# Performance work log

Hardware: AMD Instinct MI355X
Metric: run time of the kernel (lower is better)

The kernel has to match this reference:

```python
import jax, jax.numpy as jnp
import numpy as np

D_MODEL = 512
KEY_DIM = 512
VALUE_DIM = 512
N_HEADS = 8


def setup_inputs() -> dict:
    key = jax.random.key(0)
    ks = jax.random.split(key, 12)
    B, S = 8, 1024
    s = 0.02
    return {
        "input1": jax.random.normal(ks[0], (B, S, D_MODEL), jnp.float32),
        "input2": jax.random.normal(ks[1], (B, S, D_MODEL), jnp.float32),
        "input3": jax.random.normal(ks[2], (B, S, D_MODEL), jnp.float32),
        # per-head projection weights stacked over heads: [H, D, d]
        "Wq": jax.random.normal(ks[3], (N_HEADS, D_MODEL, KEY_DIM), jnp.float32) * s,
        "bq": jnp.zeros((N_HEADS, KEY_DIM), jnp.float32),
        "Wk": jax.random.normal(ks[4], (N_HEADS, D_MODEL, KEY_DIM), jnp.float32) * s,
        "bk": jnp.zeros((N_HEADS, KEY_DIM), jnp.float32),
        "Wv": jax.random.normal(ks[5], (N_HEADS, D_MODEL, VALUE_DIM), jnp.float32) * s,
        "bv": jnp.zeros((N_HEADS, VALUE_DIM), jnp.float32),
        # output projection: concat of heads (H*VALUE_DIM) -> KEY_DIM
        "Wo": jax.random.normal(ks[6], (N_HEADS * VALUE_DIM, KEY_DIM), jnp.float32) * s,
        "bo": jnp.zeros((KEY_DIM,), jnp.float32),
    }


def reference(input1, input2, input3, Wq, bq, Wk, bk, Wv, bv, Wo, bo):
    # Batched equivalent of the per-head Python loop:
    # each head: q=Dense_q(input1), k=Dense_k(input2), v=Dense_v(input3);
    # softmax(q k^T / sqrt(key_dim)) v; concat over heads; Dense w_o.
    q = jnp.einsum("bsd,hde->bhse", input1, Wq) + bq[None, :, None, :]
    k = jnp.einsum("bsd,hde->bhse", input2, Wk) + bk[None, :, None, :]
    v = jnp.einsum("bsd,hde->bhse", input3, Wv) + bv[None, :, None, :]
    scale = 1.0 / jnp.sqrt(jnp.asarray(KEY_DIM, q.dtype))
    scores = jnp.einsum("bhqe,bhke->bhqk", q, k) * scale  # [B,H,S,S]
    attn = jax.nn.softmax(scores, axis=-1)
    heads = jnp.einsum("bhqk,bhke->bhqe", attn, v)  # [B,H,S,VALUE_DIM]
    B, H, S, E = heads.shape
    concat = jnp.transpose(heads, (0, 2, 1, 3)).reshape(B, S, H * E)
    return concat @ Wo + bo
```

## Files before the change

### kernel.cpp

```cpp
#include <hip/hip_runtime.h>
#include <hip/hip_bf16.h>

#define DEV static __device__ __forceinline__

typedef float f32x4 __attribute__((ext_vector_type(4)));
typedef __bf16 b16x8 __attribute__((ext_vector_type(8)));

DEV unsigned short f2bf(float f) {
  union { __hip_bfloat16 h; unsigned short u; } cv;
  cv.h = __float2bfloat16(f);
  return cv.u;
}

DEV void gload_lds16(const unsigned short* g, unsigned short* l) {
  __builtin_amdgcn_global_load_lds(
      (__attribute__((address_space(1))) void*)g,
      (__attribute__((address_space(3))) void*)l, 16, 0, 0);
}

__global__ __launch_bounds__(256) void k_convall(
    const float* __restrict__ in1, const float* __restrict__ in2,
    const float* __restrict__ in3, const float* __restrict__ Wq,
    const float* __restrict__ Wk,
    unsigned short* __restrict__ in1b, unsigned short* __restrict__ in2b,
    unsigned short* __restrict__ in3b, unsigned short* __restrict__ wqb,
    unsigned short* __restrict__ wkb) {
  const int b = blockIdx.x;
  const float* src;
  unsigned short* dst;
  long long off;
  if (b < 4096) { src = in1; dst = in1b; off = b; }
  else if (b < 8192) { src = in2; dst = in2b; off = b - 4096; }
  else if (b < 12288) { src = in3; dst = in3b; off = b - 8192; }
  else if (b < 14336) { src = Wq; dst = wqb; off = b - 12288; }
  else { src = Wk; dst = wkb; off = b - 14336; }
  const long long i = off * 256 + threadIdx.x;
  const float4 v = ((const float4*)src)[i];
  ushort4 o;
  o.x = f2bf(v.x); o.y = f2bf(v.y); o.z = f2bf(v.z); o.w = f2bf(v.w);
  ((ushort4*)dst)[i] = o;
}

__global__ __launch_bounds__(256) void k_transall(const float* __restrict__ Wv,
                                                  const float* __restrict__ Wo,
                                                  unsigned short* __restrict__ wvt,
                                                  unsigned short* __restrict__ wot) {
  __shared__ float t[32][33];
  const int yy = blockIdx.y;
  const float* src;
  unsigned short* dst;
  long long zo;
  int R, C, r0;
  const int c0 = blockIdx.x * 32;
  if (yy < 128) {
    src = Wv; dst = wvt; R = 512; C = 512;
    zo = (long long)(yy >> 4) * 512 * 512;
    r0 = (yy & 15) * 32;
  } else {
    src = Wo; dst = wot; R = 4096; C = 512;
    zo = 0;
    r0 = (yy - 128) * 32;
  }
  const int tx = threadIdx.x & 31, ty = threadIdx.x >> 5;
#pragma unroll
  for (int i = 0; i < 4; ++i)
    t[ty + i * 8][tx] = src[zo + (long long)(r0 + ty + i * 8) * C + c0 + tx];
  __syncthreads();
#pragma unroll
  for (int i = 0; i < 4; ++i)
    dst[zo + (long long)(c0 + ty + i * 8) * R + r0 + tx] = f2bf(t[tx][ty + i * 8]);
}

__global__ __launch_bounds__(256) void k_uv(const float* __restrict__ Wq, const float* __restrict__ bk,
                                            const float* __restrict__ Wk, const float* __restrict__ bq,
                                            float* __restrict__ u, float* __restrict__ v) {
  const int sel = blockIdx.y;
  const float* W = sel ? Wk : Wq;
  const float* bb = sel ? bq : bk;
  float* dst = sel ? v : u;
  const int wave = threadIdx.x >> 6, lane = threadIdx.x & 63;
  const int idx = blockIdx.x * 4 + wave;
  const int h = idx >> 9, d = idx & 511;
  const float* wr = W + ((long long)h * 512 + d) * 512 + lane * 8;
  const float* br = bb + h * 512 + lane * 8;
  float s = 0.f;
#pragma unroll
  for (int k = 0; k < 8; ++k) s += wr[k] * br[k];
#pragma unroll
  for (int off = 32; off; off >>= 1) s += __shfl_xor(s, off);
  if (lane == 0) dst[h * 512 + d] = s;
}

__global__ __launch_bounds__(512) void k_bdot(const float* __restrict__ bq,
                                              const float* __restrict__ bk,
                                              float* __restrict__ c) {
  const int wave = threadIdx.x >> 6, lane = threadIdx.x & 63;
  const float* a = bq + wave * 512 + lane * 8;
  const float* b = bk + wave * 512 + lane * 8;
  float s = 0.f;
#pragma unroll
  for (int k = 0; k < 8; ++k) s += a[k] * b[k];
#pragma unroll
  for (int off = 32; off; off >>= 1) s += __shfl_xor(s, off);
  if (lane == 0) c[wave] = s;
}

__global__ __launch_bounds__(256) void k_rtct(const float* __restrict__ in1, const float* __restrict__ in2,
                                              const float* __restrict__ u, const float* __restrict__ v,
                                              const float* __restrict__ cbuf,
                                              float* __restrict__ rt, float* __restrict__ ct) {
  const int sel = blockIdx.y;
  const float* src = sel ? in2 : in1;
  const float* vec = sel ? v : u;
  float* dst = sel ? ct : rt;
  const int row = blockIdx.x;
  __shared__ float x[512];
  const float* p = src + (long long)row * 512;
  x[threadIdx.x] = p[threadIdx.x];
  x[threadIdx.x + 256] = p[threadIdx.x + 256];
  __syncthreads();
  const int wave = threadIdx.x >> 6, lane = threadIdx.x & 63;
  const int b = row >> 10, i = row & 1023;
#pragma unroll
  for (int t = 0; t < 2; ++t) {
    const int h = wave * 2 + t;
    const float* wv = vec + h * 512;
    float s = 0.f;
#pragma unroll
    for (int k = 0; k < 8; ++k) s += x[lane + k * 64] * wv[lane + k * 64];
#pragma unroll
    for (int off = 32; off; off >>= 1) s += __shfl_xor(s, off);
    if (lane == 0)
      dst[((long long)(b * 8 + h)) * 1024 + i] = s + (sel ? 0.f : cbuf[h]);
  }
}

__global__ __launch_bounds__(256) void k_softmax_bf16(unsigned short* __restrict__ P) {
  const int wave = threadIdx.x >> 6, lane = threadIdx.x & 63;
  unsigned short* p = P + ((long long)blockIdx.x * 4 + wave) * 1024 + lane * 16;
  const b16x8 v0 = *(const b16x8*)p;
  const b16x8 v1 = *(const b16x8*)(p + 8);
  float f[16];
#pragma unroll
  for (int j = 0; j < 8; ++j) { f[j] = (float)v0[j]; f[8 + j] = (float)v1[j]; }
  float mx = f[0];
#pragma unroll
  for (int j = 1; j < 16; ++j) mx = fmaxf(mx, f[j]);
#pragma unroll
  for (int off = 32; off; off >>= 1) mx = fmaxf(mx, __shfl_xor(mx, off));
  float sum = 0.f;
#pragma unroll
  for (int j = 0; j < 16; ++j) { f[j] = __expf(f[j] - mx); sum += f[j]; }
#pragma unroll
  for (int off = 32; off; off >>= 1) sum += __shfl_xor(sum, off);
  const float inv = 1.f / sum;
  b16x8 o0, o1;
#pragma unroll
  for (int j = 0; j < 8; ++j) { o0[j] = (__bf16)(f[j] * inv); o1[j] = (__bf16)(f[8 + j] * inv); }
  *(b16x8*)p = o0;
  *(b16x8*)(p + 8) = o1;
}

template <int OM>
__global__ __launch_bounds__(256) void k_gemm_bt(
    const unsigned short* __restrict__ A, const unsigned short* __restrict__ Bt,
    void* __restrict__ Cv, const float* __restrict__ bias,
    const float* __restrict__ rAdd, const float* __restrict__ cAdd,
    int K, int lda, int ldb, int ldc,
    int azs, int azm, long long azr,
    int bzs, int bzm, long long bzr,
    int czs, long long czr, int czm, int czc,
    int biasm, int bstr, int rstr, float scale) {
  __shared__ unsigned short lA[128 * 64];
  __shared__ unsigned short lB[128 * 64];
  const int tid = threadIdx.x, wave = tid >> 6, lane = tid & 63;
  const int z = blockIdx.z;
  const int m0 = blockIdx.y * 128, n0 = blockIdx.x * 128;
  const unsigned short* Az = A + (long long)((z >> azs) & azm) * azr + (long long)m0 * lda;
  const unsigned short* Bz = Bt + (long long)((z >> bzs) & bzm) * bzr + (long long)n0 * ldb;

  const int srow = wave * 32 + (lane >> 3);
  const int scol = (lane & 7) * 8;
  const unsigned short* ga = Az + (long long)srow * lda + scol;
  const unsigned short* gb = Bz + (long long)srow * ldb + scol;
  unsigned short* laBase = &lA[(wave * 32) * 64];
  unsigned short* lbBase = &lB[(wave * 32) * 64];

  f32x4 acc[4][4] = {};
  const int wr = (wave >> 1) * 64, wc = (wave & 1) * 64;
  const int fr = lane & 15, kq = (lane >> 4) * 8;

  for (int k0 = 0; k0 < K; k0 += 64) {
#pragma unroll
    for (int i = 0; i < 4; ++i) {
      gload_lds16(ga + (long long)(i * 8) * lda + k0, laBase + (i * 8) * 64);
      gload_lds16(gb + (long long)(i * 8) * ldb + k0, lbBase + (i * 8) * 64);
    }
    __syncthreads();
#pragma unroll
    for (int kk = 0; kk < 64; kk += 32) {
      b16x8 af[4], bf[4];
#pragma unroll
      for (int i = 0; i < 4; ++i)
        af[i] = *(const b16x8*)&lA[(wr + i * 16 + fr) * 64 + kk + kq];
#pragma unroll
      for (int j = 0; j < 4; ++j)
        bf[j] = *(const b16x8*)&lB[(wc + j * 16 + fr) * 64 + kk + kq];
#pragma unroll
      for (int i = 0; i < 4; ++i)
#pragma unroll
        for (int j = 0; j < 4; ++j)
          acc[i][j] = __builtin_amdgcn_mfma_f32_16x16x32_bf16(af[i], bf[j], acc[i][j], 0, 0, 0);
    }
    __syncthreads();
  }

  const long long coff = (long long)(z >> czs) * czr + (long long)(z & czm) * czc;
  const long long zr = (long long)z * rstr;
  const int rr = (lane >> 4) * 4;
#pragma unroll
  for (int j = 0; j < 4; ++j) {
    const int col = n0 + wc + j * 16 + fr;
    const float bval = bias ? bias[(long long)(z & biasm) * bstr + col] : 0.f;
    const float ca = cAdd ? cAdd[zr + col] : 0.f;
#pragma unroll
    for (int i = 0; i < 4; ++i) {
#pragma unroll
      for (int r = 0; r < 4; ++r) {
        const int row = m0 + wr + i * 16 + rr + r;
        const float ra = rAdd ? rAdd[zr + row] : 0.f;
        const float val = (acc[i][j][r] + ra + ca) * scale + bval;
        if constexpr (OM == 1) {
          ((unsigned short*)Cv)[coff + (long long)row * ldc + col] = f2bf(val);
        } else if constexpr (OM == 2) {
          ((unsigned short*)Cv)[coff + (long long)col * ldc + row] = f2bf(val);
        } else {
          ((float*)Cv)[coff + (long long)row * ldc + col] = val;
        }
      }
    }
  }
}

#define STAGE_A8(nb, koff, i)                                  \
  gload_lds16(gaL + (long long)((i) * 8) * lda + (koff) + scol, \
              &sh[nb][(wid * 32 + (i) * 8) * 64])
#define STAGE_B8(nb, koff, i)                                  \
  gload_lds16(gbL + (long long)((i) * 8) * ldb + (koff) + scol, \
              &sh[2 + (nb)][(wid * 32 + (i) * 8) * 64])

template <int OM>
__global__ __launch_bounds__(512, 2) void k_gemm8p(
    const unsigned short* __restrict__ A, const unsigned short* __restrict__ Bt,
    void* __restrict__ Cv, const float* __restrict__ bias,
    const float* __restrict__ rAdd, const float* __restrict__ cAdd,
    int K, int lda, int ldb, int ldc,
    int azs, int azm, long long azr,
    int bzs, int bzm, long long bzr,
    int czs, long long czr, int czm, int czc,
    int biasm, int bstr, int rstr, float scale, int kzm, int kzr) {
  __shared__ unsigned short sh[4][256 * 64];
  const int tid = threadIdx.x, wid = tid >> 6, lane = tid & 63;
  const int wm = wid >> 2, wn = wid & 3;

  const int gx = gridDim.x, gy = gridDim.y;
  const int nwg = gx * gy * gridDim.z;
  const int bidL = blockIdx.x + gx * (blockIdx.y + gy * blockIdx.z);
  const int q8 = nwg >> 3;
  const int idx = (bidL & 7) * q8 + (bidL >> 3);
  const int bx = idx % gx;
  const int rem = idx / gx;
  const int by = rem % gy;
  const int z = rem / gy;

  const int m0 = by * 256, n0 = bx * 256;
  const int kstart = (z & kzm) * kzr;
  const unsigned short* Az = A + (long long)((z >> azs) & azm) * azr + (long long)m0 * lda + kstart;
  const unsigned short* Bz = Bt + (long long)((z >> bzs) & bzm) * bzr + (long long)n0 * ldb + kstart;

  const int scol = (((lane & 7) ^ ((lane >> 3) & 7)) << 3);
  const unsigned short* gaL = Az + (long long)(wid * 32 + (lane >> 3)) * lda;
  const unsigned short* gbL = Bz + (long long)(wid * 32 + (lane >> 3)) * ldb;

  const int fr = lane & 15, kq = (lane >> 4) * 8;
  const int fsw = (fr & 7) << 3;
  const int rc0 = kq ^ fsw;
  const int rc1 = (32 + kq) ^ fsw;
  const int aBase = (wm * 128 + fr) * 64;
  const int bBase = (wn * 64 + fr) * 64;

  f32x4 acc[8][4] = {};
  b16x8 afr[4][2], bfr[4][2];
  const int NT = K >> 6;

#pragma unroll
  for (int i = 0; i < 4; ++i) { STAGE_A8(0, 0, i); STAGE_B8(0, 0, i); }

  for (int kt = 0; kt < NT; ++kt) {
    const int cur = kt & 1, nb = cur ^ 1;
    if (kt + 1 < NT) {
      const int ko = (kt + 1) << 6;
#pragma unroll
      for (int i = 0; i < 4; ++i) { STAGE_A8(nb, ko, i); STAGE_B8(nb, ko, i); }
      asm volatile("s_waitcnt vmcnt(8)" ::: "memory");
    } else {
      asm volatile("s_waitcnt vmcnt(0)" ::: "memory");
    }
    __builtin_amdgcn_s_barrier();
    __builtin_amdgcn_sched_barrier(0);

#pragma unroll
    for (int i = 0; i < 4; ++i) {
      afr[i][0] = *(const b16x8*)&sh[cur][aBase + i * 1024 + rc0];
      afr[i][1] = *(const b16x8*)&sh[cur][aBase + i * 1024 + rc1];
    }
#pragma unroll
    for (int j = 0; j < 2; ++j) {
      bfr[j][0] = *(const b16x8*)&sh[2 + cur][bBase + j * 1024 + rc0];
      bfr[j][1] = *(const b16x8*)&sh[2 + cur][bBase + j * 1024 + rc1];
    }
    __builtin_amdgcn_s_setprio(1);
#pragma unroll
    for (int t = 0; t < 2; ++t)
#pragma unroll
      for (int i = 0; i < 4; ++i)
#pragma unroll
        for (int j = 0; j < 2; ++j)
          acc[i][j] = __builtin_amdgcn_mfma_f32_16x16x32_bf16(afr[i][t], bfr[j][t], acc[i][j], 0, 0, 0);
    __builtin_amdgcn_s_setprio(0);
#pragma unroll
    for (int j = 2; j < 4; ++j) {
      bfr[j][0] = *(const b16x8*)&sh[2 + cur][bBase + j * 1024 + rc0];
      bfr[j][1] = *(const b16x8*)&sh[2 + cur][bBase + j * 1024 + rc1];
    }
    __builtin_amdgcn_s_setprio(1);
#pragma unroll
    for (int t = 0; t < 2; ++t)
#pragma unroll
      for (int i = 0; i < 4; ++i)
#pragma unroll
        for (int j = 2; j < 4; ++j)
          acc[i][j] = __builtin_amdgcn_mfma_f32_16x16x32_bf16(afr[i][t], bfr[j][t], acc[i][j], 0, 0, 0);
    __builtin_amdgcn_s_setprio(0);
#pragma unroll
    for (int i = 0; i < 4; ++i) {
      afr[i][0] = *(const b16x8*)&sh[cur][aBase + (i + 4) * 1024 + rc0];
      afr[i][1] = *(const b16x8*)&sh[cur][aBase + (i + 4) * 1024 + rc1];
    }
    __builtin_amdgcn_s_setprio(1);
#pragma unroll
    for (int t = 0; t < 2; ++t)
#pragma unroll
      for (int i = 0; i < 4; ++i)
#pragma unroll
        for (int j = 0; j < 2; ++j)
          acc[i + 4][j] = __builtin_amdgcn_mfma_f32_16x16x32_bf16(afr[i][t], bfr[j][t], acc[i + 4][j], 0, 0, 0);
    __builtin_amdgcn_s_setprio(0);
    __builtin_amdgcn_s_setprio(1);
#pragma unroll
    for (int t = 0; t < 2; ++t)
#pragma unroll
      for (int i = 0; i < 4; ++i)
#pragma unroll
        for (int j = 2; j < 4; ++j)
          acc[i + 4][j] = __builtin_amdgcn_mfma_f32_16x16x32_bf16(afr[i][t], bfr[j][t], acc[i + 4][j], 0, 0, 0);
    __builtin_amdgcn_s_setprio(0);

    __builtin_amdgcn_s_barrier();
  }

  const long long coff = (long long)(z >> czs) * czr + (long long)(z & czm) * czc;
  const long long zr = (long long)z * rstr;
  const int rr = (lane >> 4) * 4;
  unsigned short* flat = &sh[0][0];

#pragma unroll
  for (int j = 0; j < 4; ++j) {
    const int col = n0 + wn * 64 + j * 16 + fr;
    const float bval = bias ? bias[(long long)(z & biasm) * bstr + col] : 0.f;
    const float ca = cAdd ? cAdd[zr + col] : 0.f;
#pragma unroll
    for (int i = 0; i < 8; ++i) {
#pragma unroll
      for (int r = 0; r < 4; ++r) {
        const int row = m0 + wm * 128 + i * 16 + rr + r;
        const float ra = rAdd ? rAdd[zr + row] : 0.f;
        const float val = (acc[i][j][r] + ra + ca) * scale + bval;
        const int rowL = wm * 128 + i * 16 + rr + r;
        const int colL = wn * 64 + j * 16 + fr;
        const int sR = (OM == 2) ? colL : rowL;
        const int sC = (OM == 2) ? rowL : colL;
        flat[sR * 256 + (sC ^ ((sR & 7) << 3))] = f2bf(val);
      }
    }
  }
  __builtin_amdgcn_s_barrier();
  const long long rbase = (OM == 2) ? (long long)n0 : (long long)m0;
  const long long cbase = (OM == 2) ? (long long)m0 : (long long)n0;
  unsigned short* Cb = (unsigned short*)Cv;
#pragma unroll
  for (int it = 0; it < 16; ++it) {
    const int t = it * 512 + tid;
    const int R = t >> 5;
    const int Cq = t & 31;
    const int q = Cq ^ (R & 7);
    const b16x8 v = *(const b16x8*)&flat[R * 256 + q * 8];
    *(b16x8*)(Cb + coff + (rbase + R) * ldc + cbase + Cq * 8) = v;
  }
}

#define STAGE_GA(nb, koff, i)                                  \
  gload_lds16(gaL + (long long)((i) * 8) * lda + (koff) + scol, \
              &sh[nb][(wid * 32 + (i) * 8) * 64])
#define STAGE_GB(nb, koff, i)                                  \
  gload_lds16(gbL + (long long)((i) * 8) * ldb + (koff) + scol, \
              &sh[2 + (nb)][(wid * 32 + (i) * 8) * 64])

template <int OM>
__global__ __launch_bounds__(256, 2) void k_g128(
    const unsigned short* __restrict__ A, const unsigned short* __restrict__ Bt,
    void* __restrict__ Cv, const float* __restrict__ bias,
    const float* __restrict__ rAdd, const float* __restrict__ cAdd,
    int K, int lda, int ldb, int ldc,
    int azs, int azm, long long azr,
    int bzs, int bzm, long long bzr,
    int czs, long long czr, int czm, int czc,
    int biasm, int bstr, int rstr, float scale, int kzm, int kzr) {
  __shared__ unsigned short sh[4][128 * 64];
  const int tid = threadIdx.x, wid = tid >> 6, lane = tid & 63;
  const int wm = wid >> 1, wn = wid & 1;

  const int gx = gridDim.x, gy = gridDim.y;
  const int nwg = gx * gy * gridDim.z;
  const int bidL = blockIdx.x + gx * (blockIdx.y + gy * blockIdx.z);
  const int q8 = nwg >> 3;
  const int idx = (bidL & 7) * q8 + (bidL >> 3);
  const int bx = idx % gx;
  const int rem = idx / gx;
  const int by = rem % gy;
  const int z = rem / gy;

  const int m0 = by * 128, n0 = bx * 128;
  const int kstart = (z & kzm) * kzr;
  const unsigned short* Az = A + (long long)((z >> azs) & azm) * azr + (long long)m0 * lda + kstart;
  const unsigned short* Bz = Bt + (long long)((z >> bzs) & bzm) * bzr + (long long)n0 * ldb + kstart;

  const int scol = (((lane & 7) ^ ((lane >> 3) & 7)) << 3);
  const unsigned short* gaL = Az + (long long)(wid * 32 + (lane >> 3)) * lda;
  const unsigned short* gbL = Bz + (long long)(wid * 32 + (lane >> 3)) * ldb;

  const int fr = lane & 15, kq = (lane >> 4) * 8;
  const int fsw = (fr & 7) << 3;
  const int rc0 = kq ^ fsw;
  const int rc1 = (32 + kq) ^ fsw;
  const int aBase = (wm * 64 + fr) * 64;
  const int bBase = (wn * 64 + fr) * 64;

  f32x4 acc[4][4] = {};
  b16x8 afr[4][2], bfr[4][2];
  const int NT = K >> 6;

#pragma unroll
  for (int i = 0; i < 4; ++i) { STAGE_GA(0, 0, i); STAGE_GB(0, 0, i); }

  for (int kt = 0; kt < NT; ++kt) {
    const int cur = kt & 1, nb = cur ^ 1;
    if (kt + 1 < NT) {
      const int ko = (kt + 1) << 6;
#pragma unroll
      for (int i = 0; i < 4; ++i) { STAGE_GA(nb, ko, i); STAGE_GB(nb, ko, i); }
      asm volatile("s_waitcnt vmcnt(8)" ::: "memory");
    } else {
      asm volatile("s_waitcnt vmcnt(0)" ::: "memory");
    }
    __builtin_amdgcn_s_barrier();
    __builtin_amdgcn_sched_barrier(0);

#pragma unroll
    for (int i = 0; i < 4; ++i) {
      afr[i][0] = *(const b16x8*)&sh[cur][aBase + i * 1024 + rc0];
      afr[i][1] = *(const b16x8*)&sh[cur][aBase + i * 1024 + rc1];
    }
#pragma unroll
    for (int j = 0; j < 4; ++j) {
      bfr[j][0] = *(const b16x8*)&sh[2 + cur][bBase + j * 1024 + rc0];
      bfr[j][1] = *(const b16x8*)&sh[2 + cur][bBase + j * 1024 + rc1];
    }
#pragma unroll
    for (int t = 0; t < 2; ++t)
#pragma unroll
      for (int i = 0; i < 4; ++i)
#pragma unroll
        for (int j = 0; j < 4; ++j)
          acc[i][j] = __builtin_amdgcn_mfma_f32_16x16x32_bf16(afr[i][t], bfr[j][t], acc[i][j], 0, 0, 0);

    __builtin_amdgcn_s_barrier();
  }

  const long long coff = (long long)(z >> czs) * czr + (long long)(z & czm) * czc;
  const long long zr = (long long)z * rstr;
  const int rr = (lane >> 4) * 4;
  unsigned short* flat = &sh[0][0];

  if constexpr (OM == 1 || OM == 2) {
#pragma unroll
    for (int j = 0; j < 4; ++j) {
      const int col = n0 + wn * 64 + j * 16 + fr;
      const float bval = bias ? bias[(long long)(z & biasm) * bstr + col] : 0.f;
      const float ca = cAdd ? cAdd[zr + col] : 0.f;
#pragma unroll
      for (int i = 0; i < 4; ++i) {
#pragma unroll
        for (int r = 0; r < 4; ++r) {
          const int row = m0 + wm * 64 + i * 16 + rr + r;
          const float ra = rAdd ? rAdd[zr + row] : 0.f;
          const float val = (acc[i][j][r] + ra + ca) * scale + bval;
          const int rowL = wm * 64 + i * 16 + rr + r;
          const int colL = wn * 64 + j * 16 + fr;
          const int sR = (OM == 2) ? colL : rowL;
          const int sC = (OM == 2) ? rowL : colL;
          flat[sR * 128 + (sC ^ ((sR & 7) << 3))] = f2bf(val);
        }
      }
    }
    __builtin_amdgcn_s_barrier();
    const long long rbase = (OM == 2) ? (long long)n0 : (long long)m0;
    const long long cbase = (OM == 2) ? (long long)m0 : (long long)n0;
    unsigned short* Cb = (unsigned short*)Cv;
#pragma unroll
    for (int it = 0; it < 8; ++it) {
      const int t = it * 256 + tid;
      const int R = t >> 4;
      const int Cq = t & 15;
      const int q = Cq ^ (R & 7);
      const b16x8 v = *(const b16x8*)&flat[R * 128 + q * 8];
      *(b16x8*)(Cb + coff + (rbase + R) * ldc + cbase + Cq * 8) = v;
    }
  } else {
    float* fflat = (float*)flat;
    float* Cf = (float*)Cv;
#pragma unroll
    for (int j = 0; j < 4; ++j) {
      const int col = n0 + wn * 64 + j * 16 + fr;
      const float bval = bias ? bias[(long long)(z & biasm) * bstr + col] : 0.f;
      const float ca = cAdd ? cAdd[zr + col] : 0.f;
#pragma unroll
      for (int i = 0; i < 4; ++i) {
#pragma unroll
        for (int r = 0; r < 4; ++r) {
          const int row = m0 + wm * 64 + i * 16 + rr + r;
          const float ra = rAdd ? rAdd[zr + row] : 0.f;
          const float val = (acc[i][j][r] + ra + ca) * scale + bval;
          const int Rl = wm * 64 + i * 16 + rr + r;
          const int Cl = wn * 64 + j * 16 + fr;
          fflat[Rl * 128 + (Cl ^ ((Rl & 7) << 2))] = val;
        }
      }
    }
    __builtin_amdgcn_s_barrier();
#pragma unroll
    for (int it = 0; it < 16; ++it) {
      const int t = it * 256 + tid;
      const int R = t >> 5;
      const int Cq = t & 31;
      const int q = Cq ^ (R & 7);
      const float4 v = *(const float4*)&fflat[R * 128 + q * 4];
      *(float4*)(Cf + coff + (long long)(m0 + R) * ldc + n0 + Cq * 4) = v;
    }
  }
}

extern "C" void kernel_launch(void* const* d_in, const int* in_sizes, int n_in,
                              void* d_out, int out_size, void* d_ws, size_t ws_size,
                              hipStream_t stream) {
  const float* in1 = (const float*)d_in[0];
  const float* in2 = (const float*)d_in[1];
  const float* in3 = (const float*)d_in[2];
  const float* Wq = (const float*)d_in[3];
  const float* bq = (const float*)d_in[4];
  const float* Wk = (const float*)d_in[5];
  const float* bk = (const float*)d_in[6];
  const float* Wv = (const float*)d_in[7];
  const float* bv = (const float*)d_in[8];
  const float* Wo = (const float*)d_in[9];
  const float* bo = (const float*)d_in[10];

  const long long MB = 1024 * 1024;
  typedef unsigned short us;
  unsigned char* w = (unsigned char*)d_ws;
  us* in2b = (us*)(w);
  us* Tbuf = (us*)(w + 8 * MB);
  us* Vt = (us*)(w + 72 * MB);
  us* wvt = (us*)(w + 136 * MB);
  us* wot = (us*)(w + 140 * MB);
  us* scb = (us*)(w + 144 * MB);
  us* in1b = (us*)(w + 208 * MB);
  us* in3b = (us*)(w + 216 * MB);
  us* wqb = (us*)(w + 224 * MB);
  us* wkb = (us*)(w + 228 * MB);
  us* Gt = (us*)(w + 232 * MB);
  float* rt = (float*)(w + 236 * MB);
  float* ct = (float*)(w + 236 * MB + (256 << 10));
  float* ubuf = (float*)(w + 237 * MB);
  float* vbuf = (float*)(w + 237 * MB + (16 << 10));
  float* cbuf = (float*)(w + 237 * MB + (32 << 10));
  if ((long long)ws_size < 238 * MB) return;

  const float iscale = 0.04419417382415922f;
  const long long SD = 1024 * 512;

  k_convall<<<16384, 256, 0, stream>>>(in1, in2, in3, Wq, Wk,
                                       in1b, in2b, in3b, wqb, wkb);
  k_transall<<<dim3(16, 256), 256, 0, stream>>>(Wv, Wo, wvt, wot);

  k_uv<<<dim3(1024, 2), 256, 0, stream>>>(Wq, bk, Wk, bq, ubuf, vbuf);
  k_bdot<<<1, 512, 0, stream>>>(bq, bk, cbuf);
  k_rtct<<<dim3(8192, 2), 256, 0, stream>>>(in1, in2, ubuf, vbuf, cbuf, rt, ct);

  k_gemm_bt<1><<<dim3(4, 4, 8), 256, 0, stream>>>(
      wkb, wqb, Gt, nullptr, nullptr, nullptr, 512, 512, 512, 512,
      0, 7, 262144LL, 0, 7, 262144LL, 0, 262144LL, 0, 0, 0, 0, 0, 1.f);

  k_gemm8p<1><<<dim3(2, 4, 64), 512, 0, stream>>>(
      in1b, Gt, Tbuf, nullptr, nullptr, nullptr, 512, 512, 512, 512,
      3, 7, SD, 0, 7, 262144LL, 0, SD, 0, 0, 0, 0, 0, 1.f, 0, 0);

  k_gemm8p<2><<<dim3(2, 4, 64), 512, 0, stream>>>(
      in3b, wvt, Vt, bv, nullptr, nullptr, 512, 512, 512, 1024,
      3, 7, SD, 0, 7, 262144LL, 0, SD, 0, 0, 7, 512, 0, 1.f, 0, 0);

  for (int c = 0; c < 2; ++c) {
    k_gemm8p<1><<<dim3(4, 4, 32), 512, 0, stream>>>(
        Tbuf + (long long)c * 32 * SD, in2b + (long long)c * 4 * SD, scb, nullptr,
        rt + c * 32768, ct + c * 32768, 512, 512, 512, 1024,
        0, 31, SD, 3, 3, SD, 0, 1048576LL, 0, 0, 0, 0, 1024, iscale, 0, 0);
    k_softmax_bf16<<<8192, 256, 0, stream>>>(scb);
    k_gemm8p<1><<<dim3(2, 4, 32), 512, 0, stream>>>(
        scb, Vt + (long long)c * 32 * SD, Tbuf + (long long)c * 16777216LL, nullptr,
        nullptr, nullptr, 1024, 1024, 1024, 4096,
        0, 31, 1048576LL, 0, 31, SD, 3, 4194304LL, 7, 512, 0, 0, 0, 1.f, 0, 0);
  }

  k_g128<0><<<dim3(4, 64, 1), 256, 0, stream>>>(
      Tbuf, wot, d_out, bo, nullptr, nullptr, 4096, 4096, 4096, 512,
      0, 0, 0, 0, 0, 0, 0, 0, 0, 0, 0, 0, 0, 1.f, 0, 0);
}
```

Before: 465.0 us.

## Fuse QK^T, softmax and PV into a single attention kernel

Replaces the chunked sequence of score GEMM, separate bf16 softmax and PV GEMM with one k_attn kernel. Each block computes a 64-row query tile's full 1024-wide score row in registers, does a cross-wave softmax via LDS, stores the probabilities in LDS and multiplies by V, writing the concatenated head output directly. This removes the round trip of the B*H*S*S score matrix through global memory and several launches. In exchange it uses large LDS (160KB), limiting occupancy, and the PV loop loads V without double buffering.

```diff
diff --git a/kernel.cpp b/kernel.cpp
--- a/kernel.cpp
+++ b/kernel.cpp
@@ -135,32 +135,6 @@
   }
 }
 
-__global__ __launch_bounds__(256) void k_softmax_bf16(unsigned short* __restrict__ P) {
-  const int wave = threadIdx.x >> 6, lane = threadIdx.x & 63;
-  unsigned short* p = P + ((long long)blockIdx.x * 4 + wave) * 1024 + lane * 16;
-  const b16x8 v0 = *(const b16x8*)p;
-  const b16x8 v1 = *(const b16x8*)(p + 8);
-  float f[16];
-#pragma unroll
-  for (int j = 0; j < 8; ++j) { f[j] = (float)v0[j]; f[8 + j] = (float)v1[j]; }
-  float mx = f[0];
-#pragma unroll
-  for (int j = 1; j < 16; ++j) mx = fmaxf(mx, f[j]);
-#pragma unroll
-  for (int off = 32; off; off >>= 1) mx = fmaxf(mx, __shfl_xor(mx, off));
-  float sum = 0.f;
-#pragma unroll
-  for (int j = 0; j < 16; ++j) { f[j] = __expf(f[j] - mx); sum += f[j]; }
-#pragma unroll
-  for (int off = 32; off; off >>= 1) sum += __shfl_xor(sum, off);
-  const float inv = 1.f / sum;
-  b16x8 o0, o1;
-#pragma unroll
-  for (int j = 0; j < 8; ++j) { o0[j] = (__bf16)(f[j] * inv); o1[j] = (__bf16)(f[8 + j] * inv); }
-  *(b16x8*)p = o0;
-  *(b16x8*)(p + 8) = o1;
-}
-
 template <int OM>
 __global__ __launch_bounds__(256) void k_gemm_bt(
     const unsigned short* __restrict__ A, const unsigned short* __restrict__ Bt,
@@ -406,6 +380,228 @@
     const int q = Cq ^ (R & 7);
     const b16x8 v = *(const b16x8*)&flat[R * 256 + q * 8];
     *(b16x8*)(Cb + coff + (rbase + R) * ldc + cbase + Cq * 8) = v;
+  }
+}
+
+__global__ __launch_bounds__(512, 2) void k_attn(
+    const unsigned short* __restrict__ T, const unsigned short* __restrict__ X2,
+    const unsigned short* __restrict__ Vt,
+    const float* __restrict__ rt, const float* __restrict__ ct,
+    unsigned short* __restrict__ Cout, float iscale) {
+  __shared__ unsigned short sh[81920];
+  const int tid = threadIdx.x, wid = tid >> 6, lane = tid & 63;
+  const int bidL = blockIdx.x + 16 * blockIdx.y;
+  const int idx = (bidL & 7) * 128 + (bidL >> 3);
+  const int qt = idx & 15, z = idx >> 4;
+  const int b = z >> 3, h = z & 7;
+
+  const unsigned short* Tz = T + (long long)z * 524288 + (long long)qt * 64 * 512;
+  const unsigned short* Xb = X2 + (long long)b * 524288;
+  const unsigned short* Vz = Vt + (long long)z * 524288;
+
+  const int fr = lane & 15;
+  const int kq4 = lane >> 4;
+  const int rr = kq4 * 4;
+  const int srow4 = lane >> 2;
+  const int sq = (((lane & 3) ^ ((lane >> 2) & 3)) << 3);
+
+  f32x4 acc1[4][8] = {};
+  {
+#pragma unroll
+    for (int ii = 0; ii < 8; ++ii)
+      gload_lds16(Xb + (long long)(wid * 128 + ii * 16 + srow4) * 512 + sq,
+                  &sh[4096 + (wid * 128 + ii * 16) * 32 + lane * 8]);
+    if (wid < 4)
+      gload_lds16(Tz + (long long)(wid * 16 + srow4) * 512 + sq,
+                  &sh[(wid * 16) * 32 + lane * 8]);
+  }
+  for (int kt = 0; kt < 16; ++kt) {
+    const int cur = kt & 1, nb = cur ^ 1;
+    if (kt < 15) {
+      const int ko = (kt + 1) * 32;
+#pragma unroll
+      for (int ii = 0; ii < 8; ++ii)
+        gload_lds16(Xb + (long long)(wid * 128 + ii * 16 + srow4) * 512 + ko + sq,
+                    &sh[4096 + nb * 32768 + (wid * 128 + ii * 16) * 32 + lane * 8]);
+      if (wid < 4) {
+        gload_lds16(Tz + (long long)(wid * 16 + srow4) * 512 + ko + sq,
+                    &sh[nb * 2048 + (wid * 16) * 32 + lane * 8]);
+        asm volatile("s_waitcnt vmcnt(9)" ::: "memory");
+      } else {
+        asm volatile("s_waitcnt vmcnt(8)" ::: "memory");
+      }
+    } else {
+      asm volatile("s_waitcnt vmcnt(0)" ::: "memory");
+    }
+    __builtin_amdgcn_s_barrier();
+    __builtin_amdgcn_sched_barrier(0);
+    const int aB = cur * 2048, bB = 4096 + cur * 32768;
+    b16x8 af[4], bf[8];
+#pragma unroll
+    for (int i = 0; i < 4; ++i) {
+      const int row = i * 16 + fr;
+      af[i] = *(const b16x8*)&sh[aB + row * 32 + ((kq4 ^ (row & 3)) << 3)];
+    }
+#pragma unroll
+    for (int j = 0; j < 8; ++j) {
+      const int n = wid * 128 + j * 16 + fr;
+      bf[j] = *(const b16x8*)&sh[bB + n * 32 + ((kq4 ^ (n & 3)) << 3)];
+    }
+    __builtin_amdgcn_s_setprio(1);
+#pragma unroll
+    for (int i = 0; i < 4; ++i)
+#pragma unroll
+      for (int j = 0; j < 8; ++j)
+        acc1[i][j] = __builtin_amdgcn_mfma_f32_16x16x32_bf16(af[i], bf[j], acc1[i][j], 0, 0, 0);
+    __builtin_amdgcn_s_setprio(0);
+    __builtin_amdgcn_s_barrier();
+  }
+
+  float ca[8];
+#pragma unroll
+  for (int j = 0; j < 8; ++j) ca[j] = ct[(long long)z * 1024 + wid * 128 + j * 16 + fr];
+  float ra[4][4];
+#pragma unroll
+  for (int i = 0; i < 4; ++i)
+#pragma unroll
+    for (int r = 0; r < 4; ++r)
+      ra[i][r] = rt[(long long)z * 1024 + qt * 64 + i * 16 + rr + r];
+#pragma unroll
+  for (int i = 0; i < 4; ++i)
+#pragma unroll
+    for (int j = 0; j < 8; ++j)
+#pragma unroll
+      for (int r = 0; r < 4; ++r)
+        acc1[i][j][r] = (acc1[i][j][r] + ra[i][r] + ca[j]) * iscale;
+
+  float* sred = (float*)&sh[69632];
+  float* ssum = (float*)&sh[70656];
+  float rmax[4][4];
+#pragma unroll
+  for (int i = 0; i < 4; ++i)
+#pragma unroll
+    for (int r = 0; r < 4; ++r) {
+      float m = acc1[i][0][r];
+#pragma unroll
+      for (int j = 1; j < 8; ++j) m = fmaxf(m, acc1[i][j][r]);
+#pragma unroll
+      for (int off = 1; off < 16; off <<= 1) m = fmaxf(m, __shfl_xor(m, off));
+      rmax[i][r] = m;
+    }
+  if (fr == 0) {
+#pragma unroll
+    for (int i = 0; i < 4; ++i)
+#pragma unroll
+      for (int r = 0; r < 4; ++r) sred[wid * 64 + i * 16 + rr + r] = rmax[i][r];
+  }
+  __syncthreads();
+#pragma unroll
+  for (int i = 0; i < 4; ++i)
+#pragma unroll
+    for (int r = 0; r < 4; ++r) {
+      float m = sred[i * 16 + rr + r];
+#pragma unroll
+      for (int w = 1; w < 8; ++w) m = fmaxf(m, sred[w * 64 + i * 16 + rr + r]);
+      rmax[i][r] = m;
+    }
+  float rsum[4][4];
+#pragma unroll
+  for (int i = 0; i < 4; ++i)
+#pragma unroll
+    for (int r = 0; r < 4; ++r) {
+      float s = 0.f;
+#pragma unroll
+      for (int j = 0; j < 8; ++j) {
+        const float v = __expf(acc1[i][j][r] - rmax[i][r]);
+        acc1[i][j][r] = v;
+        s += v;
+      }
+#pragma unroll
+      for (int off = 1; off < 16; off <<= 1) s += __shfl_xor(s, off);
+      rsum[i][r] = s;
+    }
+  __syncthreads();
+  if (fr == 0) {
+#pragma unroll
+    for (int i = 0; i < 4; ++i)
+#pragma unroll
+      for (int r = 0; r < 4; ++r) ssum[wid * 64 + i * 16 + rr + r] = rsum[i][r];
+  }
+  __syncthreads();
+#pragma unroll
+  for (int i = 0; i < 4; ++i)
+#pragma unroll
+    for (int r = 0; r < 4; ++r) {
+      float s = ssum[i * 16 + rr + r];
+#pragma unroll
+      for (int w = 1; w < 8; ++w) s += ssum[w * 64 + i * 16 + rr + r];
+      rsum[i][r] = 1.f / s;
+    }
+#pragma unroll
+  for (int i = 0; i < 4; ++i)
+#pragma unroll
+    for (int j = 0; j < 8; ++j)
+#pragma unroll
+      for (int r = 0; r < 4; ++r) {
+        const int row = i * 16 + rr + r;
+        const int col = wid * 128 + j * 16 + fr;
+        sh[row * 1024 + ((((col >> 3) ^ (row & 7)) << 3) | (col & 7))] =
+            f2bf(acc1[i][j][r] * rsum[i][r]);
+      }
+  __syncthreads();
+
+  f32x4 acc2[4][4] = {};
+  for (int kt = 0; kt < 32; ++kt) {
+#pragma unroll
+    for (int ii = 0; ii < 4; ++ii)
+      gload_lds16(Vz + (long long)(wid * 64 + ii * 16 + srow4) * 1024 + kt * 32 + sq,
+                  &sh[65536 + (wid * 64 + ii * 16) * 32 + lane * 8]);
+    asm volatile("s_waitcnt vmcnt(0)" ::: "memory");
+    __builtin_amdgcn_s_barrier();
+    __builtin_amdgcn_sched_barrier(0);
+    b16x8 pa[4], vb[4];
+#pragma unroll
+    for (int i = 0; i < 4; ++i) {
+      const int row = i * 16 + fr;
+      const int q = kt * 4 + kq4;
+      pa[i] = *(const b16x8*)&sh[row * 1024 + ((q ^ (row & 7)) << 3)];
+    }
+#pragma unroll
+    for (int j = 0; j < 4; ++j) {
+      const int e = wid * 64 + j * 16 + fr;
+      vb[j] = *(const b16x8*)&sh[65536 + e * 32 + ((kq4 ^ (e & 3)) << 3)];
+    }
+    __builtin_amdgcn_s_setprio(1);
+#pragma unroll
+    for (int i = 0; i < 4; ++i)
+#pragma unroll
+      for (int j = 0; j < 4; ++j)
+        acc2[i][j] = __builtin_amdgcn_mfma_f32_16x16x32_bf16(pa[i], vb[j], acc2[i][j], 0, 0, 0);
+    __builtin_amdgcn_s_setprio(0);
+    __builtin_amdgcn_s_barrier();
+  }
+
+#pragma unroll
+  for (int i = 0; i < 4; ++i)
+#pragma unroll
+    for (int j = 0; j < 4; ++j)
+#pragma unroll
+      for (int r = 0; r < 4; ++r) {
+        const int row = i * 16 + rr + r;
+        const int col = wid * 64 + j * 16 + fr;
+        sh[row * 512 + ((((col >> 3) ^ (row & 7)) << 3) | (col & 7))] =
+            f2bf(acc2[i][j][r]);
+      }
+  __syncthreads();
+  unsigned short* Crow = Cout + (long long)(b * 1024 + qt * 64) * 4096 + h * 512;
+#pragma unroll
+  for (int it = 0; it < 8; ++it) {
+    const int t = it * 512 + tid;
+    const int R = t >> 6;
+    const int Cq = t & 63;
+    const int q = Cq ^ (R & 7);
+    const b16x8 v = *(const b16x8*)&sh[R * 512 + q * 8];
+    *(b16x8*)(Crow + (long long)R * 4096 + Cq * 8) = v;
   }
 }
 
@@ -629,19 +825,9 @@
       in3b, wvt, Vt, bv, nullptr, nullptr, 512, 512, 512, 1024,
       3, 7, SD, 0, 7, 262144LL, 0, SD, 0, 0, 7, 512, 0, 1.f, 0, 0);
 
-  for (int c = 0; c < 2; ++c) {
-    k_gemm8p<1><<<dim3(4, 4, 32), 512, 0, stream>>>(
-        Tbuf + (long long)c * 32 * SD, in2b + (long long)c * 4 * SD, scb, nullptr,
-        rt + c * 32768, ct + c * 32768, 512, 512, 512, 1024,
-        0, 31, SD, 3, 3, SD, 0, 1048576LL, 0, 0, 0, 0, 1024, iscale, 0, 0);
-    k_softmax_bf16<<<8192, 256, 0, stream>>>(scb);
-    k_gemm8p<1><<<dim3(2, 4, 32), 512, 0, stream>>>(
-        scb, Vt + (long long)c * 32 * SD, Tbuf + (long long)c * 16777216LL, nullptr,
-        nullptr, nullptr, 1024, 1024, 1024, 4096,
-        0, 31, 1048576LL, 0, 31, SD, 3, 4194304LL, 7, 512, 0, 0, 0, 1.f, 0, 0);
-  }
+  k_attn<<<dim3(16, 64), 512, 0, stream>>>(Tbuf, in2b, Vt, rt, ct, scb, iscale);
 
   k_g128<0><<<dim3(4, 64, 1), 256, 0, stream>>>(
-      Tbuf, wot, d_out, bo, nullptr, nullptr, 4096, 4096, 4096, 512,
+      scb, wot, d_out, bo, nullptr, nullptr, 4096, 4096, 4096, 512,
       0, 0, 0, 0, 0, 0, 0, 0, 0, 0, 0, 0, 0, 1.f, 0, 0);
 }
```

Measured after the change: 488.6 us. +5.1%, slower.

## Fold Wo into V projection and merge attention-output and output GEMMs

Applied to the files above, without the earlier changes.

Precomputes Wv_h·Wo_h per head (and bv·Wo as a bias) so each head's values are projected straight into output space. The final output becomes one GEMM over the concatenated softmax matrices (K=8192) against those pre-projected values, which removes the separate P·V GEMM and the later concat GEMM through Wo. Scores for all heads are now computed in one launch into a larger buffer, replacing the two-chunk loop. In exchange the workspace holds all heads' probabilities at once and the FLOP count changes (P·U with K=8192, N=512). The reordered product may also change bf16 rounding behaviour.

```diff
diff --git a/kernel.cpp b/kernel.cpp
--- a/kernel.cpp
+++ b/kernel.cpp
@@ -21,10 +21,10 @@
 __global__ __launch_bounds__(256) void k_convall(
     const float* __restrict__ in1, const float* __restrict__ in2,
     const float* __restrict__ in3, const float* __restrict__ Wq,
-    const float* __restrict__ Wk,
+    const float* __restrict__ Wk, const float* __restrict__ Wv,
     unsigned short* __restrict__ in1b, unsigned short* __restrict__ in2b,
     unsigned short* __restrict__ in3b, unsigned short* __restrict__ wqb,
-    unsigned short* __restrict__ wkb) {
+    unsigned short* __restrict__ wkb, unsigned short* __restrict__ wvb) {
   const int b = blockIdx.x;
   const float* src;
   unsigned short* dst;
@@ -33,7 +33,8 @@
   else if (b < 8192) { src = in2; dst = in2b; off = b - 4096; }
   else if (b < 12288) { src = in3; dst = in3b; off = b - 8192; }
   else if (b < 14336) { src = Wq; dst = wqb; off = b - 12288; }
-  else { src = Wk; dst = wkb; off = b - 14336; }
+  else if (b < 16384) { src = Wk; dst = wkb; off = b - 14336; }
+  else { src = Wv; dst = wvb; off = b - 16384; }
   const long long i = off * 256 + threadIdx.x;
   const float4 v = ((const float4*)src)[i];
   ushort4 o;
@@ -41,26 +42,12 @@
   ((ushort4*)dst)[i] = o;
 }
 
-__global__ __launch_bounds__(256) void k_transall(const float* __restrict__ Wv,
-                                                  const float* __restrict__ Wo,
-                                                  unsigned short* __restrict__ wvt,
-                                                  unsigned short* __restrict__ wot) {
+__global__ __launch_bounds__(256) void k_transpose_bf16(const float* __restrict__ src,
+                                                        unsigned short* __restrict__ dst,
+                                                        int R, int C) {
   __shared__ float t[32][33];
-  const int yy = blockIdx.y;
-  const float* src;
-  unsigned short* dst;
-  long long zo;
-  int R, C, r0;
-  const int c0 = blockIdx.x * 32;
-  if (yy < 128) {
-    src = Wv; dst = wvt; R = 512; C = 512;
-    zo = (long long)(yy >> 4) * 512 * 512;
-    r0 = (yy & 15) * 32;
-  } else {
-    src = Wo; dst = wot; R = 4096; C = 512;
-    zo = 0;
-    r0 = (yy - 128) * 32;
-  }
+  const long long zo = (long long)blockIdx.z * R * C;
+  const int c0 = blockIdx.x * 32, r0 = blockIdx.y * 32;
   const int tx = threadIdx.x & 31, ty = threadIdx.x >> 5;
 #pragma unroll
   for (int i = 0; i < 4; ++i)
@@ -133,6 +120,24 @@
     if (lane == 0)
       dst[((long long)(b * 8 + h)) * 1024 + i] = s + (sel ? 0.f : cbuf[h]);
   }
+}
+
+__global__ __launch_bounds__(256) void k_bvo(const float* __restrict__ Wo,
+                                             const float* __restrict__ bv,
+                                             float* __restrict__ bvo) {
+  const int h = blockIdx.x;
+  __shared__ float bs[512];
+  bs[threadIdx.x] = bv[h * 512 + threadIdx.x];
+  bs[threadIdx.x + 256] = bv[h * 512 + threadIdx.x + 256];
+  __syncthreads();
+  float a0 = 0.f, a1 = 0.f;
+  for (int e = 0; e < 512; ++e) {
+    const float* row = Wo + ((long long)(h * 512 + e)) * 512;
+    a0 += bs[e] * row[threadIdx.x];
+    a1 += bs[e] * row[threadIdx.x + 256];
+  }
+  bvo[h * 512 + threadIdx.x] = a0;
+  bvo[h * 512 + threadIdx.x + 256] = a1;
 }
 
 __global__ __launch_bounds__(256) void k_softmax_bf16(unsigned short* __restrict__ P) {
@@ -590,28 +595,30 @@
   unsigned char* w = (unsigned char*)d_ws;
   us* in2b = (us*)(w);
   us* Tbuf = (us*)(w + 8 * MB);
-  us* Vt = (us*)(w + 72 * MB);
-  us* wvt = (us*)(w + 136 * MB);
-  us* wot = (us*)(w + 140 * MB);
-  us* scb = (us*)(w + 144 * MB);
-  us* in1b = (us*)(w + 208 * MB);
-  us* in3b = (us*)(w + 216 * MB);
-  us* wqb = (us*)(w + 224 * MB);
-  us* wkb = (us*)(w + 228 * MB);
+  us* Ubuf = (us*)(w + 8 * MB);
+  us* Pcat = (us*)(w + 72 * MB);
+  us* in1b = (us*)(w + 200 * MB);
+  us* in3b = (us*)(w + 208 * MB);
+  us* wqb = (us*)(w + 216 * MB);
+  us* Wvot = (us*)(w + 216 * MB);
+  us* wkb = (us*)(w + 220 * MB);
+  us* wvb = (us*)(w + 224 * MB);
+  us* wotb = (us*)(w + 228 * MB);
   us* Gt = (us*)(w + 232 * MB);
   float* rt = (float*)(w + 236 * MB);
   float* ct = (float*)(w + 236 * MB + (256 << 10));
   float* ubuf = (float*)(w + 237 * MB);
   float* vbuf = (float*)(w + 237 * MB + (16 << 10));
   float* cbuf = (float*)(w + 237 * MB + (32 << 10));
+  float* bvo = (float*)(w + 237 * MB + (48 << 10));
   if ((long long)ws_size < 238 * MB) return;
 
   const float iscale = 0.04419417382415922f;
   const long long SD = 1024 * 512;
 
-  k_convall<<<16384, 256, 0, stream>>>(in1, in2, in3, Wq, Wk,
-                                       in1b, in2b, in3b, wqb, wkb);
-  k_transall<<<dim3(16, 256), 256, 0, stream>>>(Wv, Wo, wvt, wot);
+  k_convall<<<18432, 256, 0, stream>>>(in1, in2, in3, Wq, Wk, Wv,
+                                       in1b, in2b, in3b, wqb, wkb, wvb);
+  k_transpose_bf16<<<dim3(16, 128, 1), 256, 0, stream>>>(Wo, wotb, 4096, 512);
 
   k_uv<<<dim3(1024, 2), 256, 0, stream>>>(Wq, bk, Wk, bq, ubuf, vbuf);
   k_bdot<<<1, 512, 0, stream>>>(bq, bk, cbuf);
@@ -621,27 +628,26 @@
       wkb, wqb, Gt, nullptr, nullptr, nullptr, 512, 512, 512, 512,
       0, 7, 262144LL, 0, 7, 262144LL, 0, 262144LL, 0, 0, 0, 0, 0, 1.f);
 
+  k_gemm_bt<1><<<dim3(4, 4, 8), 256, 0, stream>>>(
+      wotb, wvb, Wvot, nullptr, nullptr, nullptr, 512, 4096, 512, 512,
+      0, 7, 512LL, 0, 7, 262144LL, 0, 262144LL, 0, 0, 0, 0, 0, 1.f);
+  k_bvo<<<8, 256, 0, stream>>>(Wo, bv, bvo);
+
   k_gemm8p<1><<<dim3(2, 4, 64), 512, 0, stream>>>(
       in1b, Gt, Tbuf, nullptr, nullptr, nullptr, 512, 512, 512, 512,
       3, 7, SD, 0, 7, 262144LL, 0, SD, 0, 0, 0, 0, 0, 1.f, 0, 0);
 
+  k_gemm8p<1><<<dim3(4, 4, 64), 512, 0, stream>>>(
+      Tbuf, in2b, Pcat, nullptr, rt, ct, 512, 512, 512, 8192,
+      0, 63, SD, 3, 7, SD, 3, 8388608LL, 7, 1024, 0, 0, 1024, iscale, 0, 0);
+
+  k_softmax_bf16<<<16384, 256, 0, stream>>>(Pcat);
+
   k_gemm8p<2><<<dim3(2, 4, 64), 512, 0, stream>>>(
-      in3b, wvt, Vt, bv, nullptr, nullptr, 512, 512, 512, 1024,
-      3, 7, SD, 0, 7, 262144LL, 0, SD, 0, 0, 7, 512, 0, 1.f, 0, 0);
-
-  for (int c = 0; c < 2; ++c) {
-    k_gemm8p<1><<<dim3(4, 4, 32), 512, 0, stream>>>(
-        Tbuf + (long long)c * 32 * SD, in2b + (long long)c * 4 * SD, scb, nullptr,
-        rt + c * 32768, ct + c * 32768, 512, 512, 512, 1024,
-        0, 31, SD, 3, 3, SD, 0, 1048576LL, 0, 0, 0, 0, 1024, iscale, 0, 0);
-    k_softmax_bf16<<<8192, 256, 0, stream>>>(scb);
-    k_gemm8p<1><<<dim3(2, 4, 32), 512, 0, stream>>>(
-        scb, Vt + (long long)c * 32 * SD, Tbuf + (long long)c * 16777216LL, nullptr,
-        nullptr, nullptr, 1024, 1024, 1024, 4096,
-        0, 31, 1048576LL, 0, 31, SD, 3, 4194304LL, 7, 512, 0, 0, 0, 1.f, 0, 0);
-  }
-
-  k_g128<0><<<dim3(4, 64, 1), 256, 0, stream>>>(
-      Tbuf, wot, d_out, bo, nullptr, nullptr, 4096, 4096, 4096, 512,
-      0, 0, 0, 0, 0, 0, 0, 0, 0, 0, 0, 0, 0, 1.f, 0, 0);
-}
+      in3b, Wvot, Ubuf, bvo, nullptr, nullptr, 512, 512, 512, 8192,
+      3, 7, SD, 0, 7, 262144LL, 3, 4194304LL, 7, 1024, 7, 512, 0, 1.f, 0, 0);
+
+  k_g128<0><<<dim3(4, 8, 8), 256, 0, stream>>>(
+      Pcat, Ubuf, d_out, bo, nullptr, nullptr, 8192, 8192, 8192, 512,
+      0, 7, 8388608LL, 0, 7, 4194304LL, 0, 524288LL, 0, 0, 0, 0, 0, 1.f, 0, 0);
+}
```

New measurement: 452.8 us. 2.6% less time.
